# Performance work log

Hardware: AMD Instinct MI355X
Metric: run time of the kernel (lower is better)

The kernel has to match this reference:

```python
import jax, jax.numpy as jnp
import numpy as np

N_NODES = 50000
N_EDGES = 800000
NFEAT, NHID, NCLASS = 512, 128, 64


def setup_inputs() -> dict:
    key = jax.random.key(0)
    ks = jax.random.split(key, 8)
    rows = jnp.sort(jax.random.randint(ks[1], (N_EDGES,), 0, N_NODES, dtype=jnp.int64 if jax.config.jax_enable_x64 else jnp.int32))
    cols = jax.random.randint(ks[2], (N_EDGES,), 0, N_NODES, dtype=rows.dtype)
    return {
        "x": jax.random.normal(ks[0], (N_NODES, NFEAT), dtype=jnp.float32),
        "rows": rows,
        "cols": cols,
        "vals": jax.random.uniform(ks[3], (N_EDGES,), dtype=jnp.float32),
        "W1": jax.random.normal(ks[4], (NFEAT, NHID), dtype=jnp.float32) * (1.0 / np.sqrt(NHID)),
        "b1": jax.random.normal(ks[5], (NHID,), dtype=jnp.float32) * 0.01,
        "W2": jax.random.normal(ks[6], (NHID, NCLASS), dtype=jnp.float32) * (1.0 / np.sqrt(NCLASS)),
        "b2": jax.random.normal(ks[7], (NCLASS,), dtype=jnp.float32) * 0.01,
    }


def _spmm(rows, cols, vals, h, num_nodes):
    # A @ h where A is sparse (num_nodes x num_nodes) given as COO edges.
    # Equivalent math to the custom flexspmm segmented SpMM kernel.
    msgs = vals[:, None] * h[cols]              # [E, d]
    return jax.ops.segment_sum(msgs, rows, num_segments=num_nodes)


def reference(x, rows, cols, vals, W1, b1, W2, b2):
    n = x.shape[0]
    # Layer 1: A @ (X W1) + b1   (GraphConvolution)
    h = x @ W1
    h = _spmm(rows, cols, vals, h, n) + b1
    h = jax.nn.relu(h)
    # dropout: eval mode -> identity
    # Layer 2: (A @ h) W2 + b2   (GraphConvolution2)
    h = _spmm(rows, cols, vals, h, n)
    logits = h @ W2 + b2
    return jax.nn.log_softmax(logits, axis=1)
```

## Files before the change

kernel.cpp:

```cpp
#include <hip/hip_runtime.h>
#include <hip/hip_bf16.h>
#include <math.h>


#define N_NODES 50000
#define N_EDGES 800000
#define NFEAT   512
#define NHID    128
#define NCLASS  64

typedef short  short8  __attribute__((ext_vector_type(8)));
typedef unsigned short ushort8 __attribute__((ext_vector_type(8)));
typedef float  f32x4   __attribute__((ext_vector_type(4)));

static __device__ __forceinline__ float bflo(unsigned int p) {
    return __builtin_bit_cast(float, p << 16);
}
static __device__ __forceinline__ float bfhi(unsigned int p) {
    return __builtin_bit_cast(float, p & 0xFFFF0000u);
}
static __device__ __forceinline__ unsigned short f2bf(float f) {
    unsigned int b = __builtin_bit_cast(unsigned int, f);
    return (unsigned short)((b + 0x7FFFu + ((b >> 16) & 1u)) >> 16);
}

__global__ __launch_bounds__(256) void prep_kernel(
        const float* __restrict__ W1, const float* __restrict__ W2,
        const int* __restrict__ rows,
        unsigned short* __restrict__ W1T, unsigned short* __restrict__ W2T,
        int* __restrict__ row_ptr) {
    const int tid = blockIdx.x * 256 + threadIdx.x;
    const int T   = gridDim.x * 256;
    for (int e = tid; e < N_EDGES; e += T) {
        const int re = rows[e];
        if (e == 0) {
            for (int r = 0; r <= re; ++r) row_ptr[r] = 0;
        } else {
            const int rp = rows[e - 1];
            for (int r = rp + 1; r <= re; ++r) row_ptr[r] = e;
        }
        if (e == N_EDGES - 1) {
            for (int r = re + 1; r <= N_NODES; ++r) row_ptr[r] = N_EDGES;
        }
    }
    for (int i = tid; i < NHID * NFEAT; i += T) {
        const int n = i >> 9, k = i & 511;
        W1T[i] = f2bf(W1[(size_t)k * NHID + n]);
    }
    for (int i = tid; i < NCLASS * NHID; i += T) {
        const int n = i >> 7, k = i & 127;
        W2T[i] = f2bf(W2[(size_t)k * NCLASS + n]);
    }
}

__global__ __launch_bounds__(256) void gemm1_kernel(
        const float* __restrict__ x, const unsigned short* __restrict__ W1T,
        unsigned short* __restrict__ h1b, int M) {
    __shared__ unsigned short sA[64 * 64];
    __shared__ unsigned short sB[128 * 64];

    const int tid  = threadIdx.x;
    const int lane = tid & 63;
    const int wid  = tid >> 6;
    const int wr   = wid >> 1, wc = wid & 1;
    const int row0 = blockIdx.x * 64;

    f32x4 acc[2][4];
    #pragma unroll
    for (int i = 0; i < 2; ++i)
        #pragma unroll
        for (int j = 0; j < 4; ++j)
            acc[i][j] = (f32x4){0.f, 0.f, 0.f, 0.f};

    const int arow = tid >> 2;
    const int akc  = (tid & 3) * 16;
    const int bcol = tid >> 1;
    const int bkh  = (tid & 1) * 32;

    for (int kt = 0; kt < NFEAT; kt += 64) {
        {
            float v[16];
            const float* src = x + (size_t)(row0 + arow) * NFEAT + kt + akc;
            if (row0 + arow < M) {
                #pragma unroll
                for (int i = 0; i < 4; ++i)
                    *(float4*)&v[i * 4] = *(const float4*)(src + i * 4);
            } else {
                #pragma unroll
                for (int i = 0; i < 16; ++i) v[i] = 0.f;
            }
            #pragma unroll
            for (int i2 = 0; i2 < 2; ++i2) {
                ushort8 w;
                #pragma unroll
                for (int q = 0; q < 8; ++q) w[q] = f2bf(v[i2 * 8 + q]);
                const int gran = ((akc >> 3) + i2) ^ (arow & 7);
                *(ushort8*)((char*)sA + arow * 128 + gran * 16) = w;
            }
        }
        {
            const unsigned short* srcb = W1T + (size_t)bcol * NFEAT + kt + bkh;
            #pragma unroll
            for (int i = 0; i < 4; ++i) {
                ushort8 w = *(const ushort8*)(srcb + i * 8);
                const int gran = ((bkh >> 3) + i) ^ (bcol & 7);
                *(ushort8*)((char*)sB + bcol * 128 + gran * 16) = w;
            }
        }
        __syncthreads();

        #pragma unroll
        for (int ks = 0; ks < 2; ++ks) {
            short8 af[2], bfr[4];
            #pragma unroll
            for (int i = 0; i < 2; ++i) {
                const int ar = wr * 32 + i * 16 + (lane & 15);
                const int gran = (ks * 4 + (lane >> 4)) ^ (ar & 7);
                af[i] = *(const short8*)((const char*)sA + ar * 128 + gran * 16);
            }
            #pragma unroll
            for (int j = 0; j < 4; ++j) {
                const int br = wc * 64 + j * 16 + (lane & 15);
                const int gran = (ks * 4 + (lane >> 4)) ^ (br & 7);
                bfr[j] = *(const short8*)((const char*)sB + br * 128 + gran * 16);
            }
            #pragma unroll
            for (int i = 0; i < 2; ++i)
                #pragma unroll
                for (int j = 0; j < 4; ++j)
                    acc[i][j] = __builtin_amdgcn_mfma_f32_16x16x32_bf16(
                        af[i], bfr[j], acc[i][j], 0, 0, 0);
        }
        __syncthreads();
    }

    const int cr = (lane >> 4) * 4;
    const int cc = lane & 15;
    #pragma unroll
    for (int i = 0; i < 2; ++i)
        #pragma unroll
        for (int j = 0; j < 4; ++j)
            #pragma unroll
            for (int reg = 0; reg < 4; ++reg) {
                const int row = row0 + wr * 32 + i * 16 + cr + reg;
                const int col = wc * 64 + j * 16 + cc;
                if (row < M)
                    h1b[(size_t)row * NHID + col] = f2bf(acc[i][j][reg]);
            }
}

__global__ __launch_bounds__(256) void spmm1_kernel(
        const int* __restrict__ row_ptr, const int* __restrict__ cols,
        const float* __restrict__ vals, const unsigned short* __restrict__ h1b,
        const float* __restrict__ b1, unsigned short* __restrict__ h2b,
        int nwaves) {
    const int j    = threadIdx.x & 63;
    const int wave = (blockIdx.x * 256 + threadIdx.x) >> 6;
    const float bb0 = b1[2 * j], bb1 = b1[2 * j + 1];

    for (int r = wave; r < N_NODES; r += nwaves) {
        const int lo = row_ptr[r], hi = row_ptr[r + 1];
        float a0 = 0.f, a1 = 0.f;
        int e = lo;
        for (; e + 8 <= hi; e += 8) {
            unsigned int p[8];
            float v[8];
            #pragma unroll
            for (int q = 0; q < 8; ++q) {
                const int c = cols[e + q];
                v[q] = vals[e + q];
                p[q] = *(const unsigned int*)(h1b + (size_t)c * NHID + 2 * j);
            }
            #pragma unroll
            for (int q = 0; q < 8; ++q) {
                a0 = fmaf(v[q], bflo(p[q]), a0);
                a1 = fmaf(v[q], bfhi(p[q]), a1);
            }
        }
        for (; e < hi; ++e) {
            const float vv = vals[e];
            unsigned int p = *(const unsigned int*)(h1b + (size_t)cols[e] * NHID + 2 * j);
            a0 = fmaf(vv, bflo(p), a0);
            a1 = fmaf(vv, bfhi(p), a1);
        }
        a0 += bb0; a1 += bb1;
        a0 = a0 > 0.f ? a0 : 0.f;
        a1 = a1 > 0.f ? a1 : 0.f;
        *(unsigned int*)(h2b + (size_t)r * NHID + 2 * j) =
            (unsigned int)f2bf(a0) | ((unsigned int)f2bf(a1) << 16);
    }
}

__global__ __launch_bounds__(256) void gemm2_kernel(
        const unsigned short* __restrict__ h2b,
        const unsigned short* __restrict__ W2T,
        unsigned short* __restrict__ tb, int nwaves) {
    const int lane = threadIdx.x & 63;
    const int wave = (blockIdx.x * 256 + threadIdx.x) >> 6;
    const int l15 = lane & 15, lg = lane >> 4;

    short8 Bf[4][4];
    #pragma unroll
    for (int ks = 0; ks < 4; ++ks)
        #pragma unroll
        for (int ct = 0; ct < 4; ++ct)
            Bf[ks][ct] = *(const short8*)(W2T + (size_t)(ct * 16 + l15) * NHID + ks * 32 + lg * 8);

    const int ntiles = N_NODES / 16;
    for (int t = wave; t < ntiles; t += nwaves) {
        const int r0 = t * 16;
        f32x4 acc[4];
        #pragma unroll
        for (int ct = 0; ct < 4; ++ct) acc[ct] = (f32x4){0.f, 0.f, 0.f, 0.f};
        #pragma unroll
        for (int ks = 0; ks < 4; ++ks) {
            short8 af = *(const short8*)(h2b + (size_t)(r0 + l15) * NHID + ks * 32 + lg * 8);
            #pragma unroll
            for (int ct = 0; ct < 4; ++ct)
                acc[ct] = __builtin_amdgcn_mfma_f32_16x16x32_bf16(af, Bf[ks][ct], acc[ct], 0, 0, 0);
        }
        #pragma unroll
        for (int ct = 0; ct < 4; ++ct)
            #pragma unroll
            for (int reg = 0; reg < 4; ++reg)
                tb[(size_t)(r0 + lg * 4 + reg) * NCLASS + ct * 16 + l15] = f2bf(acc[ct][reg]);
    }
}

__global__ __launch_bounds__(256) void spmm2_lsm_kernel(
        const int* __restrict__ row_ptr, const int* __restrict__ cols,
        const float* __restrict__ vals, const unsigned short* __restrict__ tb,
        const float* __restrict__ b2, float* __restrict__ out, int nwaves) {
    const int lane = threadIdx.x & 63;
    const int h = lane >> 5, j = lane & 31;
    const int wave = (blockIdx.x * 256 + threadIdx.x) >> 6;
    const float bb0 = b2[2 * j], bb1 = b2[2 * j + 1];

    for (int r = wave; r < N_NODES; r += nwaves) {
        const int lo = row_ptr[r], hi = row_ptr[r + 1];
        float a0 = 0.f, a1 = 0.f;
        int e = lo;
        for (; e + 8 <= hi; e += 8) {
            #pragma unroll
            for (int q = 0; q < 4; ++q) {
                const int ee = e + 2 * q + h;
                const float vv = vals[ee];
                unsigned int p = *(const unsigned int*)(tb + (size_t)cols[ee] * NCLASS + 2 * j);
                a0 = fmaf(vv, bflo(p), a0);
                a1 = fmaf(vv, bfhi(p), a1);
            }
        }
        for (; e + 2 <= hi; e += 2) {
            const int ee = e + h;
            const float vv = vals[ee];
            unsigned int p = *(const unsigned int*)(tb + (size_t)cols[ee] * NCLASS + 2 * j);
            a0 = fmaf(vv, bflo(p), a0);
            a1 = fmaf(vv, bfhi(p), a1);
        }
        if (e < hi && h == 0) {
            const float vv = vals[e];
            unsigned int p = *(const unsigned int*)(tb + (size_t)cols[e] * NCLASS + 2 * j);
            a0 = fmaf(vv, bflo(p), a0);
            a1 = fmaf(vv, bfhi(p), a1);
        }
        a0 += __shfl_xor(a0, 32, 64);
        a1 += __shfl_xor(a1, 32, 64);
        const float l0 = a0 + bb0, l1 = a1 + bb1;

        float m = fmaxf(l0, l1);
        #pragma unroll
        for (int off = 16; off > 0; off >>= 1)
            m = fmaxf(m, __shfl_xor(m, off, 64));
        float s = __expf(l0 - m) + __expf(l1 - m);
        #pragma unroll
        for (int off = 16; off > 0; off >>= 1)
            s += __shfl_xor(s, off, 64);
        const float ls = __logf(s);

        if (h == 0) {
            float2 o;
            o.x = (l0 - m) - ls;
            o.y = (l1 - m) - ls;
            *(float2*)(out + (size_t)r * NCLASS + 2 * j) = o;
        }
    }
}

extern "C" void kernel_launch(void* const* d_in, const int* in_sizes, int n_in,
                              void* d_out, int out_size, void* d_ws, size_t ws_size,
                              hipStream_t stream) {
    const float* x    = (const float*)d_in[0];
    const int*   rows = (const int*)  d_in[1];
    const int*   cols = (const int*)  d_in[2];
    const float* vals = (const float*)d_in[3];
    const float* W1   = (const float*)d_in[4];
    const float* b1   = (const float*)d_in[5];
    const float* W2   = (const float*)d_in[6];
    const float* b2   = (const float*)d_in[7];
    float* out = (float*)d_out;

    unsigned short* h1b = (unsigned short*)d_ws;
    unsigned short* h2b = h1b + (size_t)N_NODES * NHID;
    unsigned short* tb  = h2b + (size_t)N_NODES * NHID;
    unsigned short* W1T = tb  + (size_t)N_NODES * NCLASS;
    unsigned short* W2T = W1T + (size_t)NHID * NFEAT;
    int* row_ptr = (int*)(W2T + (size_t)NCLASS * NHID);

    const int M = N_NODES;

    prep_kernel<<<2048, 256, 0, stream>>>(W1, W2, rows, W1T, W2T, row_ptr);
    gemm1_kernel<<<(M + 63) / 64, 256, 0, stream>>>(x, W1T, h1b, M);
    spmm1_kernel<<<1024, 256, 0, stream>>>(row_ptr, cols, vals, h1b, b1, h2b, 1024 * 4);
    gemm2_kernel<<<782, 256, 0, stream>>>(h2b, W2T, tb, 782 * 4);
    spmm2_lsm_kernel<<<1024, 256, 0, stream>>>(row_ptr, cols, vals, tb, b2, out, 1024 * 4);
}
```

Measured before the change: 295.7 us.

## Split SpMM edges across lane groups with 16-byte gathers, one row per wave

```diff
diff --git a/kernel.cpp b/kernel.cpp
--- a/kernel.cpp
+++ b/kernel.cpp
@@ -13,15 +13,12 @@
 typedef unsigned short ushort8 __attribute__((ext_vector_type(8)));
 typedef float  f32x4   __attribute__((ext_vector_type(4)));
 
-static __device__ __forceinline__ float bflo(unsigned int p) {
-    return __builtin_bit_cast(float, p << 16);
-}
-static __device__ __forceinline__ float bfhi(unsigned int p) {
-    return __builtin_bit_cast(float, p & 0xFFFF0000u);
-}
 static __device__ __forceinline__ unsigned short f2bf(float f) {
     unsigned int b = __builtin_bit_cast(unsigned int, f);
     return (unsigned short)((b + 0x7FFFu + ((b >> 16) & 1u)) >> 16);
+}
+static __device__ __forceinline__ float bf2f(unsigned short u) {
+    return __builtin_bit_cast(float, ((unsigned int)u) << 16);
 }
 
 __global__ __launch_bounds__(256) void prep_kernel(
@@ -152,42 +149,64 @@
 __global__ __launch_bounds__(256) void spmm1_kernel(
         const int* __restrict__ row_ptr, const int* __restrict__ cols,
         const float* __restrict__ vals, const unsigned short* __restrict__ h1b,
-        const float* __restrict__ b1, unsigned short* __restrict__ h2b,
-        int nwaves) {
-    const int j    = threadIdx.x & 63;
-    const int wave = (blockIdx.x * 256 + threadIdx.x) >> 6;
-    const float bb0 = b1[2 * j], bb1 = b1[2 * j + 1];
-
-    for (int r = wave; r < N_NODES; r += nwaves) {
-        const int lo = row_ptr[r], hi = row_ptr[r + 1];
-        float a0 = 0.f, a1 = 0.f;
-        int e = lo;
-        for (; e + 8 <= hi; e += 8) {
-            unsigned int p[8];
-            float v[8];
-            #pragma unroll
-            for (int q = 0; q < 8; ++q) {
-                const int c = cols[e + q];
-                v[q] = vals[e + q];
-                p[q] = *(const unsigned int*)(h1b + (size_t)c * NHID + 2 * j);
-            }
-            #pragma unroll
-            for (int q = 0; q < 8; ++q) {
-                a0 = fmaf(v[q], bflo(p[q]), a0);
-                a1 = fmaf(v[q], bfhi(p[q]), a1);
-            }
-        }
-        for (; e < hi; ++e) {
-            const float vv = vals[e];
-            unsigned int p = *(const unsigned int*)(h1b + (size_t)cols[e] * NHID + 2 * j);
-            a0 = fmaf(vv, bflo(p), a0);
-            a1 = fmaf(vv, bfhi(p), a1);
-        }
-        a0 += bb0; a1 += bb1;
-        a0 = a0 > 0.f ? a0 : 0.f;
-        a1 = a1 > 0.f ? a1 : 0.f;
-        *(unsigned int*)(h2b + (size_t)r * NHID + 2 * j) =
-            (unsigned int)f2bf(a0) | ((unsigned int)f2bf(a1) << 16);
+        const float* __restrict__ b1, unsigned short* __restrict__ h2b) {
+    const int lane = threadIdx.x & 63;
+    const int g = lane >> 4;
+    const int s = lane & 15;
+    const int r = (blockIdx.x * 256 + threadIdx.x) >> 6;
+    if (r >= N_NODES) return;
+
+    const int lo = row_ptr[r], hi = row_ptr[r + 1];
+    float acc[8];
+    #pragma unroll
+    for (int q = 0; q < 8; ++q) acc[q] = 0.f;
+
+    int e = lo;
+    for (; e + 8 <= hi; e += 8) {
+        const int e0 = e + g, e1 = e + 4 + g;
+        const float v0 = __builtin_nontemporal_load(vals + e0);
+        const float v1 = __builtin_nontemporal_load(vals + e1);
+        const int   c0 = __builtin_nontemporal_load(cols + e0);
+        const int   c1 = __builtin_nontemporal_load(cols + e1);
+        const ushort8 p0 = *(const ushort8*)(h1b + (size_t)c0 * NHID + s * 8);
+        const ushort8 p1 = *(const ushort8*)(h1b + (size_t)c1 * NHID + s * 8);
+        #pragma unroll
+        for (int q = 0; q < 8; ++q) {
+            acc[q] = fmaf(v0, bf2f(p0[q]), acc[q]);
+            acc[q] = fmaf(v1, bf2f(p1[q]), acc[q]);
+        }
+    }
+    for (; e < hi; e += 4) {
+        const int ee = e + g;
+        ushort8 p = {0, 0, 0, 0, 0, 0, 0, 0};
+        float v = 0.f;
+        if (ee < hi) {
+            v = vals[ee];
+            const int c = cols[ee];
+            p = *(const ushort8*)(h1b + (size_t)c * NHID + s * 8);
+        }
+        #pragma unroll
+        for (int q = 0; q < 8; ++q)
+            acc[q] = fmaf(v, bf2f(p[q]), acc[q]);
+    }
+
+    #pragma unroll
+    for (int q = 0; q < 8; ++q) {
+        acc[q] += __shfl_xor(acc[q], 16, 64);
+        acc[q] += __shfl_xor(acc[q], 32, 64);
+    }
+
+    if (g == 0) {
+        float bv[8];
+        *(float4*)&bv[0] = *(const float4*)(b1 + s * 8);
+        *(float4*)&bv[4] = *(const float4*)(b1 + s * 8 + 4);
+        ushort8 o;
+        #pragma unroll
+        for (int q = 0; q < 8; ++q) {
+            float a = acc[q] + bv[q];
+            o[q] = f2bf(a > 0.f ? a : 0.f);
+        }
+        *(ushort8*)(h2b + (size_t)r * NHID + s * 8) = o;
     }
 }
 
@@ -230,59 +249,86 @@
 __global__ __launch_bounds__(256) void spmm2_lsm_kernel(
         const int* __restrict__ row_ptr, const int* __restrict__ cols,
         const float* __restrict__ vals, const unsigned short* __restrict__ tb,
-        const float* __restrict__ b2, float* __restrict__ out, int nwaves) {
+        const float* __restrict__ b2, float* __restrict__ out) {
     const int lane = threadIdx.x & 63;
-    const int h = lane >> 5, j = lane & 31;
-    const int wave = (blockIdx.x * 256 + threadIdx.x) >> 6;
-    const float bb0 = b2[2 * j], bb1 = b2[2 * j + 1];
-
-    for (int r = wave; r < N_NODES; r += nwaves) {
-        const int lo = row_ptr[r], hi = row_ptr[r + 1];
-        float a0 = 0.f, a1 = 0.f;
-        int e = lo;
-        for (; e + 8 <= hi; e += 8) {
-            #pragma unroll
-            for (int q = 0; q < 4; ++q) {
-                const int ee = e + 2 * q + h;
-                const float vv = vals[ee];
-                unsigned int p = *(const unsigned int*)(tb + (size_t)cols[ee] * NCLASS + 2 * j);
-                a0 = fmaf(vv, bflo(p), a0);
-                a1 = fmaf(vv, bfhi(p), a1);
-            }
-        }
-        for (; e + 2 <= hi; e += 2) {
-            const int ee = e + h;
-            const float vv = vals[ee];
-            unsigned int p = *(const unsigned int*)(tb + (size_t)cols[ee] * NCLASS + 2 * j);
-            a0 = fmaf(vv, bflo(p), a0);
-            a1 = fmaf(vv, bfhi(p), a1);
-        }
-        if (e < hi && h == 0) {
-            const float vv = vals[e];
-            unsigned int p = *(const unsigned int*)(tb + (size_t)cols[e] * NCLASS + 2 * j);
-            a0 = fmaf(vv, bflo(p), a0);
-            a1 = fmaf(vv, bfhi(p), a1);
-        }
-        a0 += __shfl_xor(a0, 32, 64);
-        a1 += __shfl_xor(a1, 32, 64);
-        const float l0 = a0 + bb0, l1 = a1 + bb1;
-
-        float m = fmaxf(l0, l1);
-        #pragma unroll
-        for (int off = 16; off > 0; off >>= 1)
-            m = fmaxf(m, __shfl_xor(m, off, 64));
-        float s = __expf(l0 - m) + __expf(l1 - m);
-        #pragma unroll
-        for (int off = 16; off > 0; off >>= 1)
-            s += __shfl_xor(s, off, 64);
-        const float ls = __logf(s);
-
-        if (h == 0) {
-            float2 o;
-            o.x = (l0 - m) - ls;
-            o.y = (l1 - m) - ls;
-            *(float2*)(out + (size_t)r * NCLASS + 2 * j) = o;
-        }
+    const int g = lane >> 3;
+    const int s = lane & 7;
+    const int r = (blockIdx.x * 256 + threadIdx.x) >> 6;
+    if (r >= N_NODES) return;
+
+    const int lo = row_ptr[r], hi = row_ptr[r + 1];
+    float acc[8];
+    #pragma unroll
+    for (int q = 0; q < 8; ++q) acc[q] = 0.f;
+
+    int e = lo;
+    for (; e + 16 <= hi; e += 16) {
+        const int e0 = e + g, e1 = e + 8 + g;
+        const float v0 = __builtin_nontemporal_load(vals + e0);
+        const float v1 = __builtin_nontemporal_load(vals + e1);
+        const int   c0 = __builtin_nontemporal_load(cols + e0);
+        const int   c1 = __builtin_nontemporal_load(cols + e1);
+        const ushort8 p0 = *(const ushort8*)(tb + (size_t)c0 * NCLASS + s * 8);
+        const ushort8 p1 = *(const ushort8*)(tb + (size_t)c1 * NCLASS + s * 8);
+        #pragma unroll
+        for (int q = 0; q < 8; ++q) {
+            acc[q] = fmaf(v0, bf2f(p0[q]), acc[q]);
+            acc[q] = fmaf(v1, bf2f(p1[q]), acc[q]);
+        }
+    }
+    for (; e < hi; e += 8) {
+        const int ee = e + g;
+        ushort8 p = {0, 0, 0, 0, 0, 0, 0, 0};
+        float v = 0.f;
+        if (ee < hi) {
+            v = vals[ee];
+            const int c = cols[ee];
+            p = *(const ushort8*)(tb + (size_t)c * NCLASS + s * 8);
+        }
+        #pragma unroll
+        for (int q = 0; q < 8; ++q)
+            acc[q] = fmaf(v, bf2f(p[q]), acc[q]);
+    }
+
+    #pragma unroll
+    for (int q = 0; q < 8; ++q) {
+        acc[q] += __shfl_xor(acc[q], 8, 64);
+        acc[q] += __shfl_xor(acc[q], 16, 64);
+        acc[q] += __shfl_xor(acc[q], 32, 64);
+    }
+
+    float l[8];
+    {
+        float bv[8];
+        *(float4*)&bv[0] = *(const float4*)(b2 + s * 8);
+        *(float4*)&bv[4] = *(const float4*)(b2 + s * 8 + 4);
+        #pragma unroll
+        for (int q = 0; q < 8; ++q) l[q] = acc[q] + bv[q];
+    }
+
+    float m = l[0];
+    #pragma unroll
+    for (int q = 1; q < 8; ++q) m = fmaxf(m, l[q]);
+    m = fmaxf(m, __shfl_xor(m, 1, 64));
+    m = fmaxf(m, __shfl_xor(m, 2, 64));
+    m = fmaxf(m, __shfl_xor(m, 4, 64));
+
+    float sum = 0.f;
+    #pragma unroll
+    for (int q = 0; q < 8; ++q) sum += __expf(l[q] - m);
+    sum += __shfl_xor(sum, 1, 64);
+    sum += __shfl_xor(sum, 2, 64);
+    sum += __shfl_xor(sum, 4, 64);
+    const float ls = __logf(sum);
+
+    if (lane < 8) {
+        float4 o0, o1;
+        o0.x = l[0] - m - ls; o0.y = l[1] - m - ls;
+        o0.z = l[2] - m - ls; o0.w = l[3] - m - ls;
+        o1.x = l[4] - m - ls; o1.y = l[5] - m - ls;
+        o1.z = l[6] - m - ls; o1.w = l[7] - m - ls;
+        *(float4*)(out + (size_t)r * NCLASS + s * 8)     = o0;
+        *(float4*)(out + (size_t)r * NCLASS + s * 8 + 4) = o1;
     }
 }
 
@@ -310,7 +356,7 @@
 
     prep_kernel<<<2048, 256, 0, stream>>>(W1, W2, rows, W1T, W2T, row_ptr);
     gemm1_kernel<<<(M + 63) / 64, 256, 0, stream>>>(x, W1T, h1b, M);
-    spmm1_kernel<<<1024, 256, 0, stream>>>(row_ptr, cols, vals, h1b, b1, h2b, 1024 * 4);
+    spmm1_kernel<<<(M * 64 + 255) / 256, 256, 0, stream>>>(row_ptr, cols, vals, h1b, b1, h2b);
     gemm2_kernel<<<782, 256, 0, stream>>>(h2b, W2T, tb, 782 * 4);
-    spmm2_lsm_kernel<<<1024, 256, 0, stream>>>(row_ptr, cols, vals, tb, b2, out, 1024 * 4);
-}
+    spmm2_lsm_kernel<<<(M * 64 + 255) / 256, 256, 0, stream>>>(row_ptr, cols, vals, tb, b2, out);
+}
```

After: 256.9 us. 1.15x faster.
